# Kernel optimization log

Measured on AMD Instinct MI355X. Metric: run time of the kernel, lower is better.

The kernel has to match this reference:

```python
import jax, jax.numpy as jnp
import numpy as np


def setup_inputs() -> dict:
    key = jax.random.key(0)
    kx, kd = jax.random.split(key)
    B, S, D = 64, 512, 384
    MAX_LEN = 2048
    x = jax.random.normal(kx, (B, S, D), dtype=jnp.float32)
    duration = jax.random.randint(kd, (B, S), 0, 8, dtype=jnp.int32)
    return {"x": x, "duration": duration, "max_len": MAX_LEN}


def reference(x, duration, max_len):
    """Vectorized length regulation.

    For output frame t of example b, the source phoneme index is
    searchsorted(cumsum(dur[b]), t, side='right'), i.e. the first phoneme
    whose cumulative duration exceeds t. Frames past min(total, max_len)
    are zero, matching the torch loop's zero-init + truncation.
    """
    B, S, D = x.shape
    # torch: nan_to_num then clamp(0, 300). Durations are ints here, so
    # only the clamp is material.
    dur = jnp.clip(duration, 0, 300).astype(jnp.int32)
    csum = jnp.cumsum(dur, axis=1)                    # [B, S]
    lengths = jnp.minimum(csum[:, -1], max_len).astype(jnp.int32)  # [B]

    t = jnp.arange(max_len, dtype=jnp.int32)          # [T]
    # idx[b, t] = index of phoneme producing output frame t
    idx = jax.vmap(lambda c: jnp.searchsorted(c, t, side='right'))(csum)  # [B, T]
    idx = jnp.clip(idx, 0, S - 1)

    out = jnp.take_along_axis(x, idx[..., None], axis=1)   # [B, T, D]
    mask = (t[None, :] < lengths[:, None])[..., None]      # [B, T, 1]
    out = jnp.where(mask, out, jnp.zeros((), dtype=x.dtype))
    return out, lengths
```

## Files before the change

kernel.cpp:

```cpp
#include <hip/hip_runtime.h>


#define TPB   512
#define TROWS 128
#define SMAX  512

typedef float f32x4 __attribute__((ext_vector_type(4)));

template <int CD4>
__global__ __launch_bounds__(TPB)
void lr_kernel(const float* __restrict__ xf, const int* __restrict__ dur,
               float* __restrict__ out, int B, int S, int T, int rtD4) {
    const int D4 = CD4 ? CD4 : rtD4;

    __shared__ int csum[SMAX];
    __shared__ int idxs[TROWS];

    const int b     = blockIdx.x;
    const int chunk = blockIdx.y;
    const int tid   = threadIdx.x;

    int dv = 0;
    if (tid < S) {
        dv = dur[(size_t)b * S + tid];
        dv = dv < 0 ? 0 : (dv > 300 ? 300 : dv);
    }
    csum[tid] = dv;
    __syncthreads();
#pragma unroll
    for (int off = 1; off < SMAX; off <<= 1) {
        int v   = csum[tid];
        int add = (tid >= off) ? csum[tid - off] : 0;
        __syncthreads();
        csum[tid] = v + add;
        __syncthreads();
    }
    const int total = csum[SMAX - 1];
    const int len   = total < T ? total : T;

    const int t0 = chunk * TROWS;
    if (tid < TROWS) {
        const int t = t0 + tid;
        int lo = 0, hi = S;
        while (lo < hi) {
            int mid = (lo + hi) >> 1;
            if (csum[mid] <= t) lo = mid + 1; else hi = mid;
        }
        idxs[tid] = lo < S ? lo : S - 1;
    }
    __syncthreads();

    const f32x4* xb = (const f32x4*)xf + (size_t)b * S * D4;
    f32x4*       ob = (f32x4*)out + ((size_t)b * T + t0) * D4;
    const int nelem = TROWS * D4;
#pragma unroll 4
    for (int e = tid; e < nelem; e += TPB) {
        const int r = e / D4;
        const int c = e - r * D4;
        const int t = t0 + r;
        f32x4 v = {0.f, 0.f, 0.f, 0.f};
        if (t < len) v = xb[(size_t)idxs[r] * D4 + c];
        if (t < T)   __builtin_nontemporal_store(v, &ob[e]);
    }

    if (chunk == 0 && tid == 0) {
        out[(size_t)B * T * (size_t)(D4 * 4) + b] = (float)len;
    }
}

extern "C" void kernel_launch(void* const* d_in, const int* in_sizes, int n_in,
                              void* d_out, int out_size, void* d_ws, size_t ws_size,
                              hipStream_t stream) {
    const float* x   = (const float*)d_in[0];
    const int*   dur = (const int*)d_in[1];
    float*       out = (float*)d_out;

    const long long n_x = in_sizes[0], n_dur = in_sizes[1];
    const int D = (int)(n_x / n_dur);
    long long B = 0, S = 0, T = 0;
    for (long long b = 1; b <= n_dur; ++b) {
        if (n_dur % b) continue;
        const long long s = n_dur / b;
        if (s > SMAX) continue;
        const long long rem = (long long)out_size - b;
        if (rem <= 0) break;
        if (rem % ((long long)D * b)) continue;
        B = b; S = s; T = rem / ((long long)D * b);
        break;
    }
    if (!B) { B = 64; S = 512; T = 2048; }

    const int D4 = D / 4;
    dim3 grid((unsigned)B, (unsigned)((T + TROWS - 1) / TROWS));
    if (D % 4 == 0 && D4 == 96) {
        lr_kernel<96><<<grid, TPB, 0, stream>>>(x, dur, out,
                                                (int)B, (int)S, (int)T, D4);
    } else if (D % 4 == 0) {
        lr_kernel<0><<<grid, TPB, 0, stream>>>(x, dur, out,
                                               (int)B, (int)S, (int)T, D4);
    }
}
```

Baseline: 47.50 us.

## Use wave-shuffle prefix scan, larger row tiles, and normal stores

The shared-memory Hillis-Steele scan, which needed two barriers per step, is replaced by a warp-shuffle scan within each 64-lane wave followed by a small cross-wave scan, cutting it to a few barriers. TROWS doubles to 256, so each block handles twice as many output rows and the per-block prefix scan is repeated half as often, at the cost of fewer blocks in the grid. Nontemporal stores become regular stores, which changes how the output writes interact with the cache.

After: 41.16 us. 1.15x faster.

```diff
diff --git a/kernel.cpp b/kernel.cpp
--- a/kernel.cpp
+++ b/kernel.cpp
@@ -2,7 +2,7 @@
 
 
 #define TPB   512
-#define TROWS 128
+#define TROWS 256
 #define SMAX  512
 
 typedef float f32x4 __attribute__((ext_vector_type(4)));
@@ -14,27 +14,42 @@
     const int D4 = CD4 ? CD4 : rtD4;
 
     __shared__ int csum[SMAX];
+    __shared__ int wsum[8];
     __shared__ int idxs[TROWS];
 
     const int b     = blockIdx.x;
     const int chunk = blockIdx.y;
     const int tid   = threadIdx.x;
+    const int lane  = tid & 63;
+    const int wave  = tid >> 6;
 
     int dv = 0;
     if (tid < S) {
         dv = dur[(size_t)b * S + tid];
         dv = dv < 0 ? 0 : (dv > 300 ? 300 : dv);
     }
-    csum[tid] = dv;
+    int v = dv;
+#pragma unroll
+    for (int off = 1; off < 64; off <<= 1) {
+        int n = __shfl_up(v, off, 64);
+        if (lane >= off) v += n;
+    }
+    if (lane == 63) wsum[wave] = v;
     __syncthreads();
+    if (wave == 0 && lane < 8) {
+        int w = wsum[lane];
 #pragma unroll
-    for (int off = 1; off < SMAX; off <<= 1) {
-        int v   = csum[tid];
-        int add = (tid >= off) ? csum[tid - off] : 0;
-        __syncthreads();
-        csum[tid] = v + add;
-        __syncthreads();
+        for (int off = 1; off < 8; off <<= 1) {
+            int n = __shfl_up(w, off, 64);
+            if (lane >= off) w += n;
+        }
+        wsum[lane] = w;
     }
+    __syncthreads();
+    if (wave > 0) v += wsum[wave - 1];
+    csum[tid] = v;
+    __syncthreads();
+
     const int total = csum[SMAX - 1];
     const int len   = total < T ? total : T;
 
@@ -58,9 +73,9 @@
         const int r = e / D4;
         const int c = e - r * D4;
         const int t = t0 + r;
-        f32x4 v = {0.f, 0.f, 0.f, 0.f};
-        if (t < len) v = xb[(size_t)idxs[r] * D4 + c];
-        if (t < T)   __builtin_nontemporal_store(v, &ob[e]);
+        f32x4 w = {0.f, 0.f, 0.f, 0.f};
+        if (t < len) w = xb[(size_t)idxs[r] * D4 + c];
+        if (t < T)   ob[e] = w;
     }
 
     if (chunk == 0 && tid == 0) {
```
